# Performance work log

Hardware: AMD Instinct MI355X
Metric: run time of the kernel (lower is better)

## Reference

```python
import jax, jax.numpy as jnp
import numpy as np

INPUT_DIM = 128
HIDDEN_DIM = 128
WINDOW_SIZE = 256
BLOCK_SIZE = 256
BATCH = 8
SEQ = 8192


def setup_inputs() -> dict:
    key = jax.random.key(0)
    ks = jax.random.split(key, 7)
    s = 1.0 / np.sqrt(INPUT_DIM)
    return {
        "x": jax.random.normal(ks[0], (BATCH, SEQ, INPUT_DIM), dtype=jnp.float32),
        "Wq": jax.random.normal(ks[1], (HIDDEN_DIM, INPUT_DIM), dtype=jnp.float32) * s,
        "bq": jax.random.normal(ks[2], (HIDDEN_DIM,), dtype=jnp.float32) * s,
        "Wk": jax.random.normal(ks[3], (HIDDEN_DIM, INPUT_DIM), dtype=jnp.float32) * s,
        "bk": jax.random.normal(ks[4], (HIDDEN_DIM,), dtype=jnp.float32) * s,
        "Wv": jax.random.normal(ks[5], (HIDDEN_DIM, INPUT_DIM), dtype=jnp.float32) * s,
        "bv": jax.random.normal(ks[6], (HIDDEN_DIM,), dtype=jnp.float32) * s,
    }


def reference(x, Wq, bq, Wk, bk, Wv, bv):
    B, S, D = x.shape
    bs, w = BLOCK_SIZE, WINDOW_SIZE
    nb = S // bs
    halo = w - 1
    W = bs + 2 * halo  # per-block K/V window width

    q = x @ Wq.T + bq  # [B,S,H]
    k = x @ Wk.T + bk
    v = x @ Wv.T + bv

    # Zero-pad K/V by halo on both sides. Since there is NO softmax, padded
    # zero keys give zero scores and padded zero values contribute zero —
    # this exactly reproduces the torch code's clamped window slicing.
    k_pad = jnp.pad(k, ((0, 0), (halo, halo), (0, 0)))
    v_pad = jnp.pad(v, ((0, 0), (halo, halo), (0, 0)))

    # Gather overlapping windows: [B, nb, W, H]
    starts = jnp.arange(nb) * bs  # window start in padded coords
    idx = starts[:, None] + jnp.arange(W)[None, :]  # [nb, W]
    k_win = k_pad[:, idx, :]
    v_win = v_pad[:, idx, :]

    q_blk = q.reshape(B, nb, bs, -1)  # [B, nb, bs, H]

    scale = 1.0 / jnp.sqrt(jnp.float32(D))
    attn = jnp.einsum('bnqh,bnkh->bnqk', q_blk, k_win) * scale  # no softmax
    out = jnp.einsum('bnqk,bnkh->bnqh', attn, v_win)
    return out.reshape(B, S, -1)
```

## Files before the change

### kernel.cpp

```cpp
#include <hip/hip_runtime.h>
#include <stdint.h>


#define B_ 8
#define S_ 8192
#define LDC 72
#define LDM 136
#define LDX 136
#define LDP 40
#define BUFB 36864
#define XOFF 73728
#define XBUF 17408

using bf16x8 = __attribute__((ext_vector_type(8))) short;
using f32x16 = __attribute__((ext_vector_type(16))) float;

__device__ __forceinline__ short f2bf(float f) {
  union { float f; uint32_t u; } v; v.f = f;
  uint32_t r = v.u + 0x7fffu + ((v.u >> 16) & 1u);
  return (short)(r >> 16);
}

__device__ __forceinline__ bf16x8 cvt8(float4 a, float4 b) {
  bf16x8 r;
  r[0] = f2bf(a.x); r[1] = f2bf(a.y); r[2] = f2bf(a.z); r[3] = f2bf(a.w);
  r[4] = f2bf(b.x); r[5] = f2bf(b.y); r[6] = f2bf(b.z); r[7] = f2bf(b.w);
  return r;
}

__global__ __launch_bounds__(512, 2) void fused_kernel(
    const float* __restrict__ x,
    const float* __restrict__ Wq, const float* __restrict__ bq,
    const float* __restrict__ Wk, const float* __restrict__ bk,
    const float* __restrict__ Wv, const float* __restrict__ bv,
    float* __restrict__ out)
{
  __shared__ __align__(16) char smem[108544];

  const int tid  = threadIdx.x;
  const int lane = tid & 63;
  const int wv   = tid >> 6;
  const int c    = lane & 31;
  const int hl   = lane >> 5;

  const int swz = (blockIdx.x & 7) * 32 + (blockIdx.x >> 3);
  const int b   = swz >> 5;
  const int n   = swz & 31;

  const int win_lo = (n == 0) ? 0 : n * 256 - 255;
  const int win_hi = (n == 31) ? S_ : n * 256 + 511;
  const int jlo    = (n == 0) ? 4 : 0;
  const int jhi    = (n == 31) ? 8 : 12;
  const int cbase  = n * 256 - 256;

  const float* xb = x + (size_t)b * S_ * 128;

  const bool is_k = (wv < 4);
  const int  pw   = wv & 3;
  const int  rt   = pw & 1;
  const int  ctp  = pw >> 1;
  const float* Wrole = is_k ? Wk : Wv;
  const float* brole = is_k ? bk : bv;

  const int sr = tid >> 3;
  const int sc = (tid & 7) << 4;

  bf16x8 wfrag[2][8];
  float  bias2[2];
  #pragma unroll
  for (int t = 0; t < 2; ++t) {
    const int ct = 2 * ctp + t;
    bias2[t] = brole[ct * 32 + c];
    const float* wr = Wrole + (size_t)(ct * 32 + c) * 128 + hl * 8;
    #pragma unroll
    for (int kst = 0; kst < 8; ++kst) {
      float4 f0 = *(const float4*)(wr + kst * 16);
      float4 f1 = *(const float4*)(wr + kst * 16 + 4);
      wfrag[t][kst] = cvt8(f0, f1);
    }
  }

  f32x16 macc[2];
  #pragma unroll
  for (int t = 0; t < 2; ++t)
    #pragma unroll
    for (int i = 0; i < 16; ++i) macc[t][i] = 0.f;

  {
    const float* xr = xb + (size_t)(cbase + jlo * 64 + sr) * 128 + sc;
    float4 f0 = ((const float4*)xr)[0], f1 = ((const float4*)xr)[1];
    float4 f2 = ((const float4*)xr)[2], f3 = ((const float4*)xr)[3];
    short* xl = (short*)(smem + XOFF);
    *(bf16x8*)(xl + sr * LDX + sc)     = cvt8(f0, f1);
    *(bf16x8*)(xl + sr * LDX + sc + 8) = cvt8(f2, f3);
  }
  __syncthreads();

  for (int j = jlo; j < jhi; ++j) {
    const int jj = j - jlo;
    const int jb = jj & 1;
    short* ktc = (short*)(smem + (size_t)jb * BUFB);
    short* vtc = ktc + 128 * LDC;
    const short* xcur = (const short*)(smem + XOFF + (size_t)jb * XBUF);
    const int c0 = cbase + j * 64;
    const bool more = (j + 1 < jhi);

    float4 fx0, fx1, fx2, fx3;
    if (more) {
      const float* xr = xb + (size_t)(c0 + 64 + sr) * 128 + sc;
      fx0 = ((const float4*)xr)[0]; fx1 = ((const float4*)xr)[1];
      fx2 = ((const float4*)xr)[2]; fx3 = ((const float4*)xr)[3];
    }

    f32x16 cacc[2];
    #pragma unroll
    for (int t = 0; t < 2; ++t)
      #pragma unroll
      for (int i = 0; i < 16; ++i) cacc[t][i] = bias2[t];
    #pragma unroll
    for (int kst = 0; kst < 8; ++kst) {
      bf16x8 a = *(const bf16x8*)(xcur + (rt * 32 + c) * LDX + kst * 16 + hl * 8);
      cacc[0] = __builtin_amdgcn_mfma_f32_32x32x16_bf16(a, wfrag[0][kst], cacc[0], 0, 0, 0);
      cacc[1] = __builtin_amdgcn_mfma_f32_32x32x16_bf16(a, wfrag[1][kst], cacc[1], 0, 0, 0);
    }

    short* dst = is_k ? ktc : vtc;
    const bool maskme = is_k && ((c0 < win_lo) | (c0 + 64 > win_hi));
    #pragma unroll
    for (int t = 0; t < 2; ++t) {
      const int d = (2 * ctp + t) * 32 + c;
      #pragma unroll
      for (int g = 0; g < 4; ++g) {
        #pragma unroll
        for (int p = 0; p < 2; ++p) {
          const int reg = g * 4 + p * 2;
          const int sl  = rt * 32 + g * 8 + hl * 4 + p * 2;
          float v0 = cacc[t][reg], v1 = cacc[t][reg + 1];
          if (maskme) {
            const int sg = c0 + sl;
            if (sg < win_lo || sg >= win_hi) v0 = 0.f;
            if (sg + 1 < win_lo || sg + 1 >= win_hi) v1 = 0.f;
          }
          const uint32_t pk = (uint32_t)(uint16_t)f2bf(v0) |
                              ((uint32_t)(uint16_t)f2bf(v1) << 16);
          *(uint32_t*)(dst + d * LDC + sl) = pk;
        }
      }
    }

    if (more) {
      short* xnx = (short*)(smem + XOFF + (size_t)(1 - jb) * XBUF);
      *(bf16x8*)(xnx + sr * LDX + sc)     = cvt8(fx0, fx1);
      *(bf16x8*)(xnx + sr * LDX + sc + 8) = cvt8(fx2, fx3);
    }
    __syncthreads();

    {
      const int ht = wv >> 1, dh = wv & 1;
      #pragma unroll
      for (int kst = 0; kst < 4; ++kst) {
        bf16x8 a = *(const bf16x8*)(vtc + (ht * 32 + c) * LDC + kst * 16 + hl * 8);
        #pragma unroll
        for (int ntl = 0; ntl < 2; ++ntl) {
          bf16x8 bb = *(const bf16x8*)(ktc + ((dh * 2 + ntl) * 32 + c) * LDC + kst * 16 + hl * 8);
          macc[ntl] = __builtin_amdgcn_mfma_f32_32x32x16_bf16(a, bb, macc[ntl], 0, 0, 0);
        }
      }
    }
  }

  short* m_l = (short*)smem;

  const float scale = 0.08838834764831845f;
  {
    const int ht = wv >> 1, dh = wv & 1;
    #pragma unroll
    for (int ntl = 0; ntl < 2; ++ntl) {
      #pragma unroll
      for (int reg = 0; reg < 16; ++reg) {
        const int row = (reg & 3) + 8 * (reg >> 2) + 4 * hl;
        m_l[(ht * 32 + row) * LDM + (dh * 2 + ntl) * 32 + c] =
            f2bf(macc[ntl][reg] * scale);
      }
    }
  }

  bf16x8 aq[8];
  {
    const float* xr = xb + (size_t)(n * 256 + wv * 32 + c) * 128 + hl * 8;
    #pragma unroll
    for (int kst = 0; kst < 8; ++kst) {
      float4 f0 = *(const float4*)(xr + kst * 16);
      float4 f1 = *(const float4*)(xr + kst * 16 + 4);
      aq[kst] = cvt8(f0, f1);
    }
  }

  __syncthreads();

  short* qpat = (short*)(smem + BUFB) + wv * (32 * LDP);
  float* opat = (float*)(smem + BUFB + 20480) + wv * (32 * 36);

  f32x16 oacc[4];
  #pragma unroll
  for (int ht = 0; ht < 4; ++ht)
    #pragma unroll
    for (int i = 0; i < 16; ++i) oacc[ht][i] = 0.f;

  #pragma unroll
  for (int nt = 0; nt < 4; ++nt) {
    bf16x8 wqf[8];
    {
      const float* wr = Wq + (size_t)(nt * 32 + c) * 128 + hl * 8;
      #pragma unroll
      for (int kst = 0; kst < 8; ++kst) {
        float4 f0 = *(const float4*)(wr + kst * 16);
        float4 f1 = *(const float4*)(wr + kst * 16 + 4);
        wqf[kst] = cvt8(f0, f1);
      }
    }
    f32x16 qacc;
    {
      const float bb = bq[nt * 32 + c];
      #pragma unroll
      for (int i = 0; i < 16; ++i) qacc[i] = bb;
    }
    #pragma unroll
    for (int kst = 0; kst < 8; ++kst)
      qacc = __builtin_amdgcn_mfma_f32_32x32x16_bf16(aq[kst], wqf[kst], qacc, 0, 0, 0);

    #pragma unroll
    for (int reg = 0; reg < 16; ++reg) {
      const int row = (reg & 3) + 8 * (reg >> 2) + 4 * hl;
      qpat[row * LDP + c] = f2bf(qacc[reg]);
    }
    #pragma unroll
    for (int kst2 = 0; kst2 < 2; ++kst2) {
      bf16x8 qf = *(const bf16x8*)(qpat + c * LDP + kst2 * 16 + hl * 8);
      #pragma unroll
      for (int ht = 0; ht < 4; ++ht) {
        bf16x8 bb = *(const bf16x8*)(m_l + (ht * 32 + c) * LDM + nt * 32 + kst2 * 16 + hl * 8);
        oacc[ht] = __builtin_amdgcn_mfma_f32_32x32x16_bf16(qf, bb, oacc[ht], 0, 0, 0);
      }
    }
  }

  float* outb = out + ((size_t)b * S_ + n * 256 + wv * 32) * 128;
  #pragma unroll
  for (int ht = 0; ht < 4; ++ht) {
    #pragma unroll
    for (int reg = 0; reg < 16; ++reg) {
      const int row = (reg & 3) + 8 * (reg >> 2) + 4 * hl;
      opat[row * 36 + c] = oacc[ht][reg];
    }
    #pragma unroll
    for (int p = 0; p < 4; ++p) {
      const int row = p * 8 + (lane >> 3);
      float4 vv = *(const float4*)(opat + row * 36 + (lane & 7) * 4);
      *(float4*)(outb + (size_t)row * 128 + ht * 32 + (lane & 7) * 4) = vv;
    }
  }
}

extern "C" void kernel_launch(void* const* d_in, const int* in_sizes, int n_in,
                              void* d_out, int out_size, void* d_ws, size_t ws_size,
                              hipStream_t stream) {
  const float* x  = (const float*)d_in[0];
  const float* Wq = (const float*)d_in[1];
  const float* bq = (const float*)d_in[2];
  const float* Wk = (const float*)d_in[3];
  const float* bk = (const float*)d_in[4];
  const float* Wv = (const float*)d_in[5];
  const float* bv = (const float*)d_in[6];
  float* out = (float*)d_out;

  fused_kernel<<<256, 512, 0, stream>>>(x, Wq, bq, Wk, bk, Wv, bv, out);
}
```

Baseline: 135.2 us.

## Accumulate windowed Gram matrix of augmented x and project by Wv/Wk afterwards

Instead of projecting every window chunk to K and V and accumulating V^T K per chunk, the kernel accumulates the symmetric Gram matrix of the masked, bias-augmented x window (x plus an indicator column). Only upper-triangle tiles are computed and mirrored. Wv and Wk with their biases are applied once at the end through two small GEMMs. This removes the per-chunk K/V projection MFMAs and halves the Gram work through symmetry. In exchange it adds an identity-MFMA transpose at staging, extra end-of-kernel GEMMs with more syncs, and an extra bf16 rounding of the Gram matrix and intermediate product.

Measured after the change: 139.2 us. 2.9% more time.

```diff
diff --git a/kernel.cpp b/kernel.cpp
--- a/kernel.cpp
+++ b/kernel.cpp
@@ -4,14 +4,15 @@
 
 #define B_ 8
 #define S_ 8192
-#define LDC 72
-#define LDM 136
-#define LDX 136
-#define LDP 40
-#define BUFB 36864
-#define XOFF 73728
-#define XBUF 17408
-
+#define LDT 68
+#define LDG 164
+#define LDM 132
+#define LDQP 36
+#define XTB 21760
+#define GOFF 43520
+#define SMEMSZ 96000
+
+using bf16x4 = __attribute__((ext_vector_type(4))) short;
 using bf16x8 = __attribute__((ext_vector_type(8))) short;
 using f32x16 = __attribute__((ext_vector_type(16))) float;
 
@@ -26,6 +27,12 @@
   r[0] = f2bf(a.x); r[1] = f2bf(a.y); r[2] = f2bf(a.z); r[3] = f2bf(a.w);
   r[4] = f2bf(b.x); r[5] = f2bf(b.y); r[6] = f2bf(b.z); r[7] = f2bf(b.w);
   return r;
+}
+
+__device__ __forceinline__ bf16x8 ld8(const short* p) {
+  bf16x4 lo = *(const bf16x4*)p;
+  bf16x4 hi = *(const bf16x4*)(p + 4);
+  return __builtin_shufflevector(lo, hi, 0, 1, 2, 3, 4, 5, 6, 7);
 }
 
 __global__ __launch_bounds__(512, 2) void fused_kernel(
@@ -35,7 +42,7 @@
     const float* __restrict__ Wv, const float* __restrict__ bv,
     float* __restrict__ out)
 {
-  __shared__ __align__(16) char smem[108544];
+  __shared__ __align__(16) char smem[SMEMSZ];
 
   const int tid  = threadIdx.x;
   const int lane = tid & 63;
@@ -55,135 +62,134 @@
 
   const float* xb = x + (size_t)b * S_ * 128;
 
-  const bool is_k = (wv < 4);
-  const int  pw   = wv & 3;
-  const int  rt   = pw & 1;
-  const int  ctp  = pw >> 1;
-  const float* Wrole = is_k ? Wk : Wv;
-  const float* brole = is_k ? bk : bv;
-
-  const int sr = tid >> 3;
-  const int sc = (tid & 7) << 4;
-
-  bf16x8 wfrag[2][8];
-  float  bias2[2];
-  #pragma unroll
-  for (int t = 0; t < 2; ++t) {
-    const int ct = 2 * ctp + t;
-    bias2[t] = brole[ct * 32 + c];
-    const float* wr = Wrole + (size_t)(ct * 32 + c) * 128 + hl * 8;
-    #pragma unroll
-    for (int kst = 0; kst < 8; ++kst) {
-      float4 f0 = *(const float4*)(wr + kst * 16);
-      float4 f1 = *(const float4*)(wr + kst * 16 + 4);
-      wfrag[t][kst] = cvt8(f0, f1);
-    }
-  }
-
-  f32x16 macc[2];
-  #pragma unroll
-  for (int t = 0; t < 2; ++t)
-    #pragma unroll
-    for (int i = 0; i < 16; ++i) macc[t][i] = 0.f;
-
-  {
-    const float* xr = xb + (size_t)(cbase + jlo * 64 + sr) * 128 + sc;
+  bf16x8 ib[2];
+  #pragma unroll
+  for (int kst = 0; kst < 2; ++kst)
+    #pragma unroll
+    for (int j = 0; j < 8; ++j)
+      ib[kst][j] = (kst * 16 + hl * 8 + j == c) ? (short)0x3F80 : (short)0;
+
+  const int st = wv >> 2, dt = wv & 3;
+
+  int t0i, t0j, t1i, t1j;
+  switch (wv) {
+    case 0: t0i=0; t0j=0; t1i=0; t1j=4; break;
+    case 1: t0i=1; t0j=1; t1i=1; t1j=4; break;
+    case 2: t0i=2; t0j=2; t1i=2; t1j=4; break;
+    case 3: t0i=3; t0j=3; t1i=3; t1j=4; break;
+    case 4: t0i=0; t0j=1; t1i=4; t1j=4; break;
+    case 5: t0i=0; t0j=2; t1i=1; t1j=2; break;
+    case 6: t0i=0; t0j=3; t1i=1; t1j=3; break;
+    default:t0i=2; t0j=3; t1i=2; t1j=3; break;
+  }
+  const bool two = (wv != 7);
+
+  {
+    int* z0 = (int*)((short*)smem + 129 * LDT);
+    int* z1 = (int*)((short*)(smem + XTB) + 129 * LDT);
+    for (int i = tid; i < 1054; i += 512) { z0[i] = 0; z1[i] = 0; }
+  }
+
+  f32x16 gacc0, gacc1;
+  #pragma unroll
+  for (int i = 0; i < 16; ++i) { gacc0[i] = 0.f; gacc1[i] = 0.f; }
+
+  auto stageWrite = [&](int c0, short* xt, float4 f0, float4 f1, float4 f2, float4 f3) {
+    bf16x8 a0 = cvt8(f0, f1), a1 = cvt8(f2, f3);
+    f32x16 cc;
+    #pragma unroll
+    for (int i = 0; i < 16; ++i) cc[i] = 0.f;
+    cc = __builtin_amdgcn_mfma_f32_32x32x16_bf16(a0, ib[0], cc, 0, 0, 0);
+    cc = __builtin_amdgcn_mfma_f32_32x32x16_bf16(a1, ib[1], cc, 0, 0, 0);
+    const bool mk = (c0 < win_lo) | (c0 + 64 > win_hi);
+    short* dst = xt + (dt * 32 + c) * LDT;
+    #pragma unroll
+    for (int g = 0; g < 4; ++g) {
+      #pragma unroll
+      for (int p = 0; p < 2; ++p) {
+        const int reg = g * 4 + p * 2;
+        const int sl  = st * 32 + g * 8 + hl * 4 + p * 2;
+        float v0 = cc[reg], v1 = cc[reg + 1];
+        if (mk) {
+          const int sg = c0 + sl;
+          if (sg < win_lo || sg >= win_hi) v0 = 0.f;
+          if (sg + 1 < win_lo || sg + 1 >= win_hi) v1 = 0.f;
+        }
+        const uint32_t pk = (uint32_t)(uint16_t)f2bf(v0) |
+                            ((uint32_t)(uint16_t)f2bf(v1) << 16);
+        *(uint32_t*)(dst + sl) = pk;
+      }
+    }
+    if (tid < 32) {
+      const int s0g = c0 + 2 * tid;
+      const uint32_t m0 = (s0g >= win_lo && s0g < win_hi) ? 0x3F80u : 0u;
+      const uint32_t m1 = (s0g + 1 >= win_lo && s0g + 1 < win_hi) ? 0x3F80u : 0u;
+      *(uint32_t*)(xt + 128 * LDT + 2 * tid) = m0 | (m1 << 16);
+    }
+  };
+
+  {
+    const float* xr = xb + (size_t)(cbase + jlo * 64 + st * 32 + c) * 128 + dt * 32 + hl * 8;
     float4 f0 = ((const float4*)xr)[0], f1 = ((const float4*)xr)[1];
-    float4 f2 = ((const float4*)xr)[2], f3 = ((const float4*)xr)[3];
-    short* xl = (short*)(smem + XOFF);
-    *(bf16x8*)(xl + sr * LDX + sc)     = cvt8(f0, f1);
-    *(bf16x8*)(xl + sr * LDX + sc + 8) = cvt8(f2, f3);
+    float4 f2 = *(const float4*)(xr + 16), f3 = *(const float4*)(xr + 20);
+    stageWrite(cbase + jlo * 64, (short*)smem, f0, f1, f2, f3);
   }
   __syncthreads();
 
   for (int j = jlo; j < jhi; ++j) {
-    const int jj = j - jlo;
-    const int jb = jj & 1;
-    short* ktc = (short*)(smem + (size_t)jb * BUFB);
-    short* vtc = ktc + 128 * LDC;
-    const short* xcur = (const short*)(smem + XOFF + (size_t)jb * XBUF);
-    const int c0 = cbase + j * 64;
+    const int jb = (j - jlo) & 1;
+    const short* xcur = (const short*)(smem + (size_t)jb * XTB);
+    short* xnxt = (short*)(smem + (size_t)(1 - jb) * XTB);
     const bool more = (j + 1 < jhi);
 
-    float4 fx0, fx1, fx2, fx3;
+    float4 f0, f1, f2, f3;
     if (more) {
-      const float* xr = xb + (size_t)(c0 + 64 + sr) * 128 + sc;
-      fx0 = ((const float4*)xr)[0]; fx1 = ((const float4*)xr)[1];
-      fx2 = ((const float4*)xr)[2]; fx3 = ((const float4*)xr)[3];
-    }
-
-    f32x16 cacc[2];
-    #pragma unroll
-    for (int t = 0; t < 2; ++t)
-      #pragma unroll
-      for (int i = 0; i < 16; ++i) cacc[t][i] = bias2[t];
-    #pragma unroll
-    for (int kst = 0; kst < 8; ++kst) {
-      bf16x8 a = *(const bf16x8*)(xcur + (rt * 32 + c) * LDX + kst * 16 + hl * 8);
-      cacc[0] = __builtin_amdgcn_mfma_f32_32x32x16_bf16(a, wfrag[0][kst], cacc[0], 0, 0, 0);
-      cacc[1] = __builtin_amdgcn_mfma_f32_32x32x16_bf16(a, wfrag[1][kst], cacc[1], 0, 0, 0);
-    }
-
-    short* dst = is_k ? ktc : vtc;
-    const bool maskme = is_k && ((c0 < win_lo) | (c0 + 64 > win_hi));
-    #pragma unroll
-    for (int t = 0; t < 2; ++t) {
-      const int d = (2 * ctp + t) * 32 + c;
-      #pragma unroll
-      for (int g = 0; g < 4; ++g) {
+      const float* xr = xb + (size_t)(cbase + (j + 1) * 64 + st * 32 + c) * 128 + dt * 32 + hl * 8;
+      f0 = ((const float4*)xr)[0]; f1 = ((const float4*)xr)[1];
+      f2 = *(const float4*)(xr + 16); f3 = *(const float4*)(xr + 20);
+    }
+
+    #pragma unroll
+    for (int kst = 0; kst < 4; ++kst) {
+      const int ko = kst * 16 + hl * 8;
+      bf16x8 a0 = ld8(xcur + (t0i * 32 + c) * LDT + ko);
+      bf16x8 b0 = ld8(xcur + (t0j * 32 + c) * LDT + ko);
+      gacc0 = __builtin_amdgcn_mfma_f32_32x32x16_bf16(a0, b0, gacc0, 0, 0, 0);
+      bf16x8 a1 = ld8(xcur + (t1i * 32 + c) * LDT + ko);
+      bf16x8 b1 = ld8(xcur + (t1j * 32 + c) * LDT + ko);
+      gacc1 = __builtin_amdgcn_mfma_f32_32x32x16_bf16(a1, b1, gacc1, 0, 0, 0);
+    }
+
+    if (more) stageWrite(cbase + (j + 1) * 64, xnxt, f0, f1, f2, f3);
+    __syncthreads();
+  }
+
+  short* gl = (short*)(smem + GOFF);
+  const float scale = 0.08838834764831845f;
+
+  auto gwrite = [&](f32x16& g, int ti, int tj) {
+    #pragma unroll
+    for (int reg = 0; reg < 16; ++reg) {
+      const int row = ti * 32 + (reg & 3) + 8 * (reg >> 2) + 4 * hl;
+      gl[row * LDG + tj * 32 + c] = f2bf(g[reg] * scale);
+    }
+    if (ti != tj) {
+      short* dst = gl + (tj * 32 + c) * LDG + ti * 32;
+      #pragma unroll
+      for (int g4 = 0; g4 < 4; ++g4) {
         #pragma unroll
         for (int p = 0; p < 2; ++p) {
-          const int reg = g * 4 + p * 2;
-          const int sl  = rt * 32 + g * 8 + hl * 4 + p * 2;
-          float v0 = cacc[t][reg], v1 = cacc[t][reg + 1];
-          if (maskme) {
-            const int sg = c0 + sl;
-            if (sg < win_lo || sg >= win_hi) v0 = 0.f;
-            if (sg + 1 < win_lo || sg + 1 >= win_hi) v1 = 0.f;
-          }
-          const uint32_t pk = (uint32_t)(uint16_t)f2bf(v0) |
-                              ((uint32_t)(uint16_t)f2bf(v1) << 16);
-          *(uint32_t*)(dst + d * LDC + sl) = pk;
+          const int reg = g4 * 4 + p * 2;
+          const int rl  = g4 * 8 + hl * 4 + p * 2;
+          const uint32_t pk = (uint32_t)(uint16_t)f2bf(g[reg] * scale) |
+                              ((uint32_t)(uint16_t)f2bf(g[reg + 1] * scale) << 16);
+          *(uint32_t*)(dst + rl) = pk;
         }
       }
     }
-
-    if (more) {
-      short* xnx = (short*)(smem + XOFF + (size_t)(1 - jb) * XBUF);
-      *(bf16x8*)(xnx + sr * LDX + sc)     = cvt8(fx0, fx1);
-      *(bf16x8*)(xnx + sr * LDX + sc + 8) = cvt8(fx2, fx3);
-    }
-    __syncthreads();
-
-    {
-      const int ht = wv >> 1, dh = wv & 1;
-      #pragma unroll
-      for (int kst = 0; kst < 4; ++kst) {
-        bf16x8 a = *(const bf16x8*)(vtc + (ht * 32 + c) * LDC + kst * 16 + hl * 8);
-        #pragma unroll
-        for (int ntl = 0; ntl < 2; ++ntl) {
-          bf16x8 bb = *(const bf16x8*)(ktc + ((dh * 2 + ntl) * 32 + c) * LDC + kst * 16 + hl * 8);
-          macc[ntl] = __builtin_amdgcn_mfma_f32_32x32x16_bf16(a, bb, macc[ntl], 0, 0, 0);
-        }
-      }
-    }
-  }
-
-  short* m_l = (short*)smem;
-
-  const float scale = 0.08838834764831845f;
-  {
-    const int ht = wv >> 1, dh = wv & 1;
-    #pragma unroll
-    for (int ntl = 0; ntl < 2; ++ntl) {
-      #pragma unroll
-      for (int reg = 0; reg < 16; ++reg) {
-        const int row = (reg & 3) + 8 * (reg >> 2) + 4 * hl;
-        m_l[(ht * 32 + row) * LDM + (dh * 2 + ntl) * 32 + c] =
-            f2bf(macc[ntl][reg] * scale);
-      }
-    }
-  }
+  };
+  gwrite(gacc0, t0i, t0j);
+  if (two) gwrite(gacc1, t1i, t1j);
 
   bf16x8 aq[8];
   {
@@ -195,11 +201,101 @@
       aq[kst] = cvt8(f0, f1);
     }
   }
-
   __syncthreads();
 
-  short* qpat = (short*)(smem + BUFB) + wv * (32 * LDP);
-  float* opat = (float*)(smem + BUFB + 20480) + wv * (32 * 36);
+  short* pl = (short*)smem;
+  {
+    const int ht = wv & 3;
+    const bool lo = (wv < 4);
+    const int nd1 = lo ? 3 : 2;
+    const int d1b = lo ? 0 : 3;
+    const int hr = ht * 32 + c;
+    bf16x8 av[9];
+    {
+      const float* wr = Wv + (size_t)hr * 128 + hl * 8;
+      #pragma unroll
+      for (int kst = 0; kst < 8; ++kst) {
+        float4 f0 = *(const float4*)(wr + kst * 16);
+        float4 f1 = *(const float4*)(wr + kst * 16 + 4);
+        av[kst] = cvt8(f0, f1);
+      }
+      bf16x8 a8 = {};
+      if (hl == 0) a8[0] = f2bf(bv[hr]);
+      av[8] = a8;
+    }
+    f32x16 pacc[3];
+    #pragma unroll
+    for (int t = 0; t < 3; ++t)
+      #pragma unroll
+      for (int i = 0; i < 16; ++i) pacc[t][i] = 0.f;
+    #pragma unroll
+    for (int t = 0; t < 3; ++t) {
+      if (t < nd1) {
+        const int d1t = d1b + t;
+        #pragma unroll
+        for (int kst = 0; kst < 9; ++kst) {
+          bf16x8 bb = ld8(gl + (d1t * 32 + c) * LDG + kst * 16 + hl * 8);
+          pacc[t] = __builtin_amdgcn_mfma_f32_32x32x16_bf16(av[kst], bb, pacc[t], 0, 0, 0);
+        }
+      }
+    }
+    #pragma unroll
+    for (int t = 0; t < 3; ++t) {
+      if (t < nd1) {
+        const int d1t = d1b + t;
+        #pragma unroll
+        for (int reg = 0; reg < 16; ++reg) {
+          const int row = ht * 32 + (reg & 3) + 8 * (reg >> 2) + 4 * hl;
+          pl[row * LDG + d1t * 32 + c] = f2bf(pacc[t][reg]);
+        }
+      }
+    }
+  }
+  __syncthreads();
+
+  short* m_l = gl;
+  {
+    const int ht = wv >> 1;
+    const int dt0 = (wv & 1) * 2;
+    bf16x8 ap[9];
+    {
+      const short* pr = pl + (ht * 32 + c) * LDG + hl * 8;
+      #pragma unroll
+      for (int kst = 0; kst < 9; ++kst) ap[kst] = ld8(pr + kst * 16);
+    }
+    f32x16 m2[2];
+    #pragma unroll
+    for (int t = 0; t < 2; ++t)
+      #pragma unroll
+      for (int i = 0; i < 16; ++i) m2[t][i] = 0.f;
+    #pragma unroll
+    for (int t = 0; t < 2; ++t) {
+      const int dr = (dt0 + t) * 32 + c;
+      const float* wr = Wk + (size_t)dr * 128 + hl * 8;
+      #pragma unroll
+      for (int kst = 0; kst < 8; ++kst) {
+        float4 f0 = *(const float4*)(wr + kst * 16);
+        float4 f1 = *(const float4*)(wr + kst * 16 + 4);
+        bf16x8 bb = cvt8(f0, f1);
+        m2[t] = __builtin_amdgcn_mfma_f32_32x32x16_bf16(ap[kst], bb, m2[t], 0, 0, 0);
+      }
+      bf16x8 b8 = {};
+      if (hl == 0) b8[0] = f2bf(bk[dr]);
+      m2[t] = __builtin_amdgcn_mfma_f32_32x32x16_bf16(ap[8], b8, m2[t], 0, 0, 0);
+    }
+    #pragma unroll
+    for (int t = 0; t < 2; ++t) {
+      #pragma unroll
+      for (int reg = 0; reg < 16; ++reg) {
+        const int row = ht * 32 + (reg & 3) + 8 * (reg >> 2) + 4 * hl;
+        m_l[row * LDM + (dt0 + t) * 32 + c] = f2bf(m2[t][reg]);
+      }
+    }
+  }
+  __syncthreads();
+
+  short* qpat = (short*)(smem + GOFF + 33792) + wv * (32 * LDQP);
+  float* opat = (float*)smem + wv * (32 * 36);
 
   f32x16 oacc[4];
   #pragma unroll
@@ -228,18 +324,17 @@
     #pragma unroll
     for (int kst = 0; kst < 8; ++kst)
       qacc = __builtin_amdgcn_mfma_f32_32x32x16_bf16(aq[kst], wqf[kst], qacc, 0, 0, 0);
-
     #pragma unroll
     for (int reg = 0; reg < 16; ++reg) {
       const int row = (reg & 3) + 8 * (reg >> 2) + 4 * hl;
-      qpat[row * LDP + c] = f2bf(qacc[reg]);
+      qpat[row * LDQP + c] = f2bf(qacc[reg]);
     }
     #pragma unroll
     for (int kst2 = 0; kst2 < 2; ++kst2) {
-      bf16x8 qf = *(const bf16x8*)(qpat + c * LDP + kst2 * 16 + hl * 8);
+      bf16x8 qf = ld8(qpat + c * LDQP + kst2 * 16 + hl * 8);
       #pragma unroll
       for (int ht = 0; ht < 4; ++ht) {
-        bf16x8 bb = *(const bf16x8*)(m_l + (ht * 32 + c) * LDM + nt * 32 + kst2 * 16 + hl * 8);
+        bf16x8 bb = ld8(m_l + (ht * 32 + c) * LDM + nt * 32 + kst2 * 16 + hl * 8);
         oacc[ht] = __builtin_amdgcn_mfma_f32_32x32x16_bf16(qf, bb, oacc[ht], 0, 0, 0);
       }
     }
```
